# Optimization experiments

Hardware: AMD Instinct MI355X
Metric: run time of the kernel (lower is better)

## Reference

```python
import jax, jax.numpy as jnp
import numpy as np

D = 128      # d_model
H = 8        # heads
HD = D // H  # head dim
FF = 1024    # feedforward
L = 6        # encoder layers
LN_EPS = 1e-5


def setup_inputs() -> dict:
    key = jax.random.key(0)
    ks = jax.random.split(key, 10)
    S, B = 512, 64
    p = lambda k, shape: jax.random.normal(k, shape, dtype=jnp.float32) * 0.02
    return {
        "src": jax.random.normal(ks[0], (S, B, D), dtype=jnp.float32),
        "Wqkv": p(ks[1], (L, 3 * D, D)), "bqkv": p(ks[2], (L, 3 * D)),
        "Wo": p(ks[3], (L, D, D)), "bo": p(ks[4], (L, D)),
        "ln1_g": jnp.ones((L, D), jnp.float32), "ln1_b": jnp.zeros((L, D), jnp.float32),
        "W1": p(ks[5], (L, FF, D)), "b1": p(ks[6], (L, FF)),
        "W2": p(ks[7], (L, D, FF)), "b2": p(ks[8], (L, D)),
        "ln2_g": jnp.ones((L, D), jnp.float32), "ln2_b": jnp.zeros((L, D), jnp.float32),
    }


def _layer_norm(x, g, b):
    mu = jnp.mean(x, axis=-1, keepdims=True)
    var = jnp.mean(jnp.square(x - mu), axis=-1, keepdims=True)
    return (x - mu) * jax.lax.rsqrt(var + LN_EPS) * g + b


def _pairwise_cos(x):
    # x: (B, S, D) -> clamped cosine similarity (B, S, S); single batched GEMM
    n = jnp.linalg.norm(x, axis=-1)                      # (B, S)
    sim = jnp.einsum('bid,bjd->bij', x, x) / (n[:, :, None] * n[:, None, :])
    return jnp.maximum(sim, 1e-6)


def _encoder_layer(x, Wqkv, bqkv, Wo, bo, g1, b1ln, W1, b1, W2, b2, g2, b2ln):
    # x: (B, S, D); PyTorch post-norm TransformerEncoderLayer (ReLU), eval mode (no dropout)
    B, S, _ = x.shape
    qkv = x @ Wqkv.T + bqkv                              # (B, S, 3D)
    q, k, v = jnp.split(qkv, 3, axis=-1)
    q = q.reshape(B, S, H, HD)
    k = k.reshape(B, S, H, HD)
    v = v.reshape(B, S, H, HD)
    scores = jnp.einsum('bqhd,bkhd->bhqk', q, k) / np.float32(np.sqrt(HD))
    attn = jax.nn.softmax(scores, axis=-1)
    o = jnp.einsum('bhqk,bkhd->bqhd', attn, v).reshape(B, S, D)
    o = o @ Wo.T + bo
    x = _layer_norm(x + o, g1, b1ln)
    ff = jax.nn.relu(x @ W1.T + b1) @ W2.T + b2
    return _layer_norm(x + ff, g2, b2ln)


def reference(src, Wqkv, bqkv, Wo, bo, ln1_g, ln1_b, W1, b1, W2, b2, ln2_g, ln2_b):
    x_bsd = jnp.transpose(src, (1, 0, 2))                # (B, S, D)
    cs = _pairwise_cos(x_bsd)
    h = x_bsd
    for i in range(L):
        h = _encoder_layer(h, Wqkv[i], bqkv[i], Wo[i], bo[i], ln1_g[i], ln1_b[i],
                           W1[i], b1[i], W2[i], b2[i], ln2_g[i], ln2_b[i])
    mask = jax.nn.sigmoid(h)
    out = mask * x_bsd
    out = out / jnp.maximum(jnp.linalg.norm(out, axis=-1, keepdims=True), 1e-12)
    sim = _pairwise_cos(out) + cs
    return jnp.clip(sim * 0.5, 0.1, 0.9)
```

## Files before the change

### kernel.cpp

```cpp
#include <hip/hip_runtime.h>
#include <cstdint>
#include <cstddef>

#define SS 512
#define BB 64
#define DD 128
#define HH 8
#define HDIM 16
#define FFD 1024
#define NL 6

typedef short bf16x8 __attribute__((ext_vector_type(8)));
typedef float f32x4 __attribute__((ext_vector_type(4)));

__device__ inline uint32_t pack2(float a, float b) {
  uint32_t r;
  asm("v_cvt_pk_bf16_f32 %0, %1, %2" : "=v"(r) : "v"(a), "v"(b));
  return r;
}

#define QSCALE 0.36067376022224085f

__global__ __launch_bounds__(256) void cvt_kernel(const float* __restrict__ s,
                                                  short* __restrict__ d, int n2) {
  int i = blockIdx.x * 256 + threadIdx.x;
  if (i < n2) {
    float2 v = ((const float2*)s)[i];
    ((uint32_t*)d)[i] = pack2(v.x, v.y);
  }
}

__global__ __launch_bounds__(256) void cvt_qkv_kernel(const float* __restrict__ s,
                                                      short* __restrict__ d) {
  int i = blockIdx.x * 256 + threadIdx.x;
  if (i < NL * 384 * 64) {
    const int within = i % (384 * 64);
    const float sc = (within < 128 * 64) ? QSCALE : 1.0f;
    float2 v = ((const float2*)s)[i];
    ((uint32_t*)d)[i] = pack2(v.x * sc, v.y * sc);
  }
}

__global__ __launch_bounds__(256) void scale_bq_kernel(const float* __restrict__ s,
                                                       float* __restrict__ d) {
  int i = blockIdx.x * 256 + threadIdx.x;
  if (i < NL * 384) {
    const float sc = ((i % 384) < 128) ? QSCALE : 1.0f;
    d[i] = s[i] * sc;
  }
}

__global__ __launch_bounds__(256) void transpose_rn_kernel(const float* __restrict__ src,
                                                           float* __restrict__ x0,
                                                           float* __restrict__ h,
                                                           short* __restrict__ hb,
                                                           short* __restrict__ xn) {
  const int wave = threadIdx.x >> 6;
  const int lane = threadIdx.x & 63;
  const int row = blockIdx.x * 4 + wave;
  const int b = row >> 9;
  const int s = row & 511;
  const float2 v = ((const float2*)(src + ((size_t)s * BB + b) * DD))[lane];
  ((float2*)(x0 + (size_t)row * DD))[lane] = v;
  ((float2*)(h + (size_t)row * DD))[lane] = v;
  ((uint32_t*)hb)[(size_t)row * 64 + lane] = pack2(v.x, v.y);
  float ss = v.x * v.x + v.y * v.y;
  #pragma unroll
  for (int off = 1; off < 64; off <<= 1) ss += __shfl_xor(ss, off);
  const float r = rsqrtf(ss);
  ((uint32_t*)xn)[(size_t)row * 64 + lane] = pack2(v.x * r, v.y * r);
}

__global__ __launch_bounds__(256) void mgemm_qkv(const short* __restrict__ Ab,
                                                 const short* __restrict__ Bw,
                                                 const float* __restrict__ bias,
                                                 short* __restrict__ Cb) {
  __shared__ uint32_t Xs[128 * 32];
  __shared__ uint32_t Wls[128 * 32];
  const int t = threadIdx.x;
  const int wave = t >> 6, lane = t & 63;
  const int g = lane >> 4, p = lane & 15;
  const int wr = wave >> 1, wc = wave & 1;
  const int m0 = blockIdx.y * 128, n0 = blockIdx.x * 128;
  const int K = DD;

  f32x4 acc[4][4];
  #pragma unroll
  for (int i = 0; i < 4; ++i)
    #pragma unroll
    for (int j = 0; j < 4; ++j) acc[i][j] = (f32x4){0.f, 0.f, 0.f, 0.f};

  for (int kt = 0; kt < K; kt += 64) {
    __syncthreads();
    #pragma unroll
    for (int i = 0; i < 4; ++i) {
      const int idx = t + i * 256;
      const int row = idx >> 3, kc = idx & 7;
      const uint4 w = *(const uint4*)(Ab + (size_t)(m0 + row) * K + kt + kc * 8);
      *(uint4*)(Xs + row * 32 + ((kc ^ (row & 7)) << 2)) = w;
      const uint4 u = *(const uint4*)(Bw + (size_t)(n0 + row) * K + kt + kc * 8);
      *(uint4*)(Wls + row * 32 + ((kc ^ (row & 7)) << 2)) = u;
    }
    __syncthreads();
    #pragma unroll
    for (int kc32 = 0; kc32 < 2; ++kc32) {
      bf16x8 xf[4], wf[4];
      #pragma unroll
      for (int mi = 0; mi < 4; ++mi) {
        const int row = wr * 64 + mi * 16 + p;
        union { bf16x8 v; uint4 w; } u;
        u.w = *(const uint4*)(Xs + row * 32 + (((kc32 * 4 + g) ^ (row & 7)) << 2));
        xf[mi] = u.v;
      }
      #pragma unroll
      for (int ni = 0; ni < 4; ++ni) {
        const int row = wc * 64 + ni * 16 + p;
        union { bf16x8 v; uint4 w; } u;
        u.w = *(const uint4*)(Wls + row * 32 + (((kc32 * 4 + g) ^ (row & 7)) << 2));
        wf[ni] = u.v;
      }
      #pragma unroll
      for (int mi = 0; mi < 4; ++mi)
        #pragma unroll
        for (int ni = 0; ni < 4; ++ni)
          acc[mi][ni] = __builtin_amdgcn_mfma_f32_16x16x32_bf16(wf[ni], xf[mi], acc[mi][ni], 0, 0, 0);
    }
  }

  #pragma unroll
  for (int mi = 0; mi < 4; ++mi) {
    const int m = m0 + wr * 64 + mi * 16 + p;
    #pragma unroll
    for (int ni = 0; ni < 4; ++ni) {
      const int nb = n0 + wc * 64 + ni * 16 + g * 4;
      const float4 bv = *(const float4*)(bias + nb);
      float c[4];
      c[0] = acc[mi][ni][0] + bv.x;
      c[1] = acc[mi][ni][1] + bv.y;
      c[2] = acc[mi][ni][2] + bv.z;
      c[3] = acc[mi][ni][3] + bv.w;
      const int bb2 = m >> 9, s = m & 511;
      const int which = nb >> 7, hh = (nb >> 4) & 7, d = nb & 15;
      uint2 w;
      w.x = pack2(c[0], c[1]);
      w.y = pack2(c[2], c[3]);
      *(uint2*)(Cb + ((((size_t)(bb2 * 3 + which) * 8 + hh) * 512 + s) * 16 + d)) = w;
    }
  }
}

__global__ __launch_bounds__(256) void cos2_kernel(const short* __restrict__ xn,
                                                   const short* __restrict__ yn,
                                                   float* __restrict__ out) {
  __shared__ uint32_t Js[128 * 64];
  const int t = threadIdx.x;
  const int w = t >> 6, lane = t & 63;
  const int g = lane >> 4, p = lane & 15;
  const int j0 = blockIdx.x * 128;
  const int i0 = blockIdx.y * 64;
  const int b = blockIdx.z;
  const short* xb = xn + (size_t)b * SS * DD;
  const short* yb = yn + (size_t)b * SS * DD;
  const int i = i0 + w * 16 + p;

  bf16x8 af[4];
  #pragma unroll
  for (int kc = 0; kc < 4; ++kc) {
    union { bf16x8 v; uint4 u; } uu;
    uu.u = *(const uint4*)(xb + (size_t)i * DD + kc * 32 + g * 8);
    af[kc] = uu.v;
  }
  #pragma unroll
  for (int q = 0; q < 8; ++q) {
    const int idx = q * 256 + t;
    const int row = idx >> 4, slot = idx & 15;
    const int key = (row & 3) | ((row >> 1) & 12);
    const uint4 u = *(const uint4*)(xb + (size_t)(j0 + row) * DD + slot * 8);
    *(uint4*)(&Js[row * 64 + ((slot ^ key) << 2)]) = u;
  }
  __syncthreads();

  f32x4 acc[8];
  #pragma unroll
  for (int q = 0; q < 8; ++q) acc[q] = (f32x4){0.f, 0.f, 0.f, 0.f};
  #pragma unroll
  for (int kc = 0; kc < 4; ++kc) {
    #pragma unroll
    for (int ni = 0; ni < 8; ++ni) {
      const int row = ni * 16 + p;
      const int key = (row & 3) | ((row >> 1) & 12);
      union { bf16x8 v; uint4 u; } jf;
      jf.u = *(const uint4*)(&Js[row * 64 + (((kc * 4 + g) ^ key) << 2)]);
      acc[ni] = __builtin_amdgcn_mfma_f32_16x16x32_bf16(jf.v, af[kc], acc[ni], 0, 0, 0);
    }
  }
  float prev[8][4];
  #pragma unroll
  for (int ni = 0; ni < 8; ++ni)
    #pragma unroll
    for (int r = 0; r < 4; ++r) prev[ni][r] = fmaxf(acc[ni][r], 1e-6f);
  __syncthreads();

  #pragma unroll
  for (int kc = 0; kc < 4; ++kc) {
    union { bf16x8 v; uint4 u; } uu;
    uu.u = *(const uint4*)(yb + (size_t)i * DD + kc * 32 + g * 8);
    af[kc] = uu.v;
  }
  #pragma unroll
  for (int q = 0; q < 8; ++q) {
    const int idx = q * 256 + t;
    const int row = idx >> 4, slot = idx & 15;
    const int key = (row & 3) | ((row >> 1) & 12);
    const uint4 u = *(const uint4*)(yb + (size_t)(j0 + row) * DD + slot * 8);
    *(uint4*)(&Js[row * 64 + ((slot ^ key) << 2)]) = u;
  }
  __syncthreads();

  #pragma unroll
  for (int q = 0; q < 8; ++q) acc[q] = (f32x4){0.f, 0.f, 0.f, 0.f};
  #pragma unroll
  for (int kc = 0; kc < 4; ++kc) {
    #pragma unroll
    for (int ni = 0; ni < 8; ++ni) {
      const int row = ni * 16 + p;
      const int key = (row & 3) | ((row >> 1) & 12);
      union { bf16x8 v; uint4 u; } jf;
      jf.u = *(const uint4*)(&Js[row * 64 + (((kc * 4 + g) ^ key) << 2)]);
      acc[ni] = __builtin_amdgcn_mfma_f32_16x16x32_bf16(jf.v, af[kc], acc[ni], 0, 0, 0);
    }
  }

  float* ob = out + (size_t)b * SS * SS;
  #pragma unroll
  for (int ni = 0; ni < 8; ++ni) {
    const int j = j0 + ni * 16 + g * 4;
    float4 wv;
    float* pw = &wv.x;
    #pragma unroll
    for (int r = 0; r < 4; ++r) {
      const float v = fmaxf(acc[ni][r], 1e-6f);
      pw[r] = fminf(fmaxf(0.5f * (v + prev[ni][r]), 0.1f), 0.9f);
    }
    *(float4*)(ob + (size_t)i * SS + j) = wv;
  }
}

__global__ __launch_bounds__(256) void wo_ffn_ln_kernel(const short* __restrict__ att,
                                                        const short* __restrict__ Wob,
                                                        const float* __restrict__ bov,
                                                        const float* __restrict__ lng1,
                                                        const float* __restrict__ lnb1,
                                                        const short* __restrict__ W1b,
                                                        const float* __restrict__ b1v,
                                                        const short* __restrict__ W2b,
                                                        const float* __restrict__ b2v,
                                                        const float* __restrict__ lng2,
                                                        const float* __restrict__ lnb2,
                                                        float* __restrict__ hx,
                                                        short* __restrict__ hb,
                                                        const float* __restrict__ x0p,
                                                        short* __restrict__ ynp) {
  __shared__ uint32_t S[10240];
  uint32_t* WoLS = S;
  uint32_t* Tb   = S;
  uint32_t* W1base = S;
  uint32_t* W2base = S + 4096;
  const int t = threadIdx.x;
  const int w = t >> 6, lane = t & 63;
  const int g = lane >> 4, p = lane & 15;
  const int m0 = blockIdx.x * 64;
  const int m = m0 + w * 16 + p;
  const int lr = w * 16 + p;
  const int lkey = (lr & 3) | ((lr >> 1) & 12);

  bf16x8 af[4];
  #pragma unroll
  for (int kc = 0; kc < 4; ++kc) {
    union { bf16x8 v; uint4 u; } uu;
    uu.u = *(const uint4*)(att + (size_t)m * DD + kc * 32 + g * 8);
    af[kc] = uu.v;
  }
  #pragma unroll
  for (int i = 0; i < 8; ++i) {
    const int idx = i * 256 + t;
    const int row = idx >> 4, slot = idx & 15;
    const int key = (row & 3) | ((row >> 1) & 12);
    const uint4 u = *(const uint4*)(Wob + (size_t)row * DD + slot * 8);
    *(uint4*)(&WoLS[row * 64 + ((slot ^ key) << 2)]) = u;
  }
  __syncthreads();

  f32x4 acc[8];
  #pragma unroll
  for (int i = 0; i < 8; ++i) acc[i] = (f32x4){0.f, 0.f, 0.f, 0.f};
  #pragma unroll
  for (int kc = 0; kc < 4; ++kc) {
    #pragma unroll
    for (int ni = 0; ni < 8; ++ni) {
      const int row = ni * 16 + p;
      const int key = (row & 3) | ((row >> 1) & 12);
      union { bf16x8 v; uint4 u; } wf;
      wf.u = *(const uint4*)(&WoLS[row * 64 + (((kc * 4 + g) ^ key) << 2)]);
      acc[ni] = __builtin_amdgcn_mfma_f32_16x16x32_bf16(wf.v, af[kc], acc[ni], 0, 0, 0);
    }
  }

  float h1r[8][4];
  float s1r = 0.0f, s2r = 0.0f;
  #pragma unroll
  for (int ni = 0; ni < 8; ++ni) {
    const int nb = ni * 16 + g * 4;
    const float4 rv = *(const float4*)(hx + (size_t)m * DD + nb);
    const float4 bv = *(const float4*)(bov + nb);
    h1r[ni][0] = acc[ni][0] + bv.x + rv.x;
    h1r[ni][1] = acc[ni][1] + bv.y + rv.y;
    h1r[ni][2] = acc[ni][2] + bv.z + rv.z;
    h1r[ni][3] = acc[ni][3] + bv.w + rv.w;
    #pragma unroll
    for (int r = 0; r < 4; ++r) {
      s1r += h1r[ni][r];
      s2r += h1r[ni][r] * h1r[ni][r];
    }
  }
  s1r += __shfl_xor(s1r, 16); s1r += __shfl_xor(s1r, 32);
  s2r += __shfl_xor(s2r, 16); s2r += __shfl_xor(s2r, 32);
  {
    const float mu = s1r * (1.0f / 128.0f);
    const float rs = rsqrtf(fmaxf(s2r * (1.0f / 128.0f) - mu * mu, 0.0f) + 1e-5f);
    #pragma unroll
    for (int ni = 0; ni < 8; ++ni) {
      const int nb = ni * 16 + g * 4;
      const float4 gv = *(const float4*)(lng1 + nb);
      const float4 bv = *(const float4*)(lnb1 + nb);
      h1r[ni][0] = (h1r[ni][0] - mu) * rs * gv.x + bv.x;
      h1r[ni][1] = (h1r[ni][1] - mu) * rs * gv.y + bv.y;
      h1r[ni][2] = (h1r[ni][2] - mu) * rs * gv.z + bv.z;
      h1r[ni][3] = (h1r[ni][3] - mu) * rs * gv.w + bv.w;
    }
  }
  __syncthreads();

  #pragma unroll
  for (int ni = 0; ni < 8; ++ni) {
    const int w16 = ni * 8 + 2 * g;
    const int slot = w16 >> 2, offs = w16 & 3;
    uint2 pk;
    pk.x = pack2(h1r[ni][0], h1r[ni][1]);
    pk.y = pack2(h1r[ni][2], h1r[ni][3]);
    *(uint2*)(&Tb[lr * 64 + ((slot ^ lkey) << 2) + offs]) = pk;
  }
  __syncthreads();

  bf16x8 hsf[4];
  #pragma unroll
  for (int kc = 0; kc < 4; ++kc) {
    union { bf16x8 v; uint4 u; } uu;
    uu.u = *(const uint4*)(&Tb[lr * 64 + (((kc * 4 + g) ^ lkey) << 2)]);
    hsf[kc] = uu.v;
  }
  __syncthreads();

  uint4 rA0, rA1, rB0, rB1;

#define FFN_LOAD(c)                                                               \
  {                                                                               \
    const int nf0_ = (c) * 32;                                                    \
    rA0 = *(const uint4*)(W1b + (size_t)(nf0_ + (t >> 4)) * DD + (t & 15) * 8);   \
    rA1 = *(const uint4*)(W1b + (size_t)(nf0_ + 16 + (t >> 4)) * DD + (t & 15) * 8); \
    rB0 = *(const uint4*)(W2b + (size_t)(t >> 2) * FFD + nf0_ + (t & 3) * 8);     \
    rB1 = *(const uint4*)(W2b + (size_t)(64 + (t >> 2)) * FFD + nf0_ + (t & 3) * 8); \
  }

#define FFN_WRITE(bufA, bufB)                                                     \
  {                                                                               \
    uint32_t* W1p = W1base + (bufA) * 2048;                                       \
    uint32_t* W2p = W2base + (bufB) * 2048;                                       \
    const int rw0 = t >> 4, sl0 = t & 15;                                         \
    const int k0 = (rw0 & 3) | ((rw0 >> 1) & 12);                                 \
    *(uint4*)(&W1p[rw0 * 64 + ((sl0 ^ k0) << 2)]) = rA0;                          \
    const int rw1 = 16 + rw0;                                                     \
    const int k1 = (rw1 & 3) | ((rw1 >> 1) & 12);                                 \
    *(uint4*)(&W1p[rw1 * 64 + ((sl0 ^ k1) << 2)]) = rA1;                          \
    const int rw2 = t >> 2, sl2 = t & 3;                                          \
    *(uint4*)(&W2p[rw2 * 16 + ((sl2 ^ ((rw2 >> 1) & 3)) << 2)]) = rB0;            \
    const int rw3 = 64 + rw2;                                                     \
    *(uint4*)(&W2p[rw3 * 16 + ((sl2 ^ ((rw3 >> 1) & 3)) << 2)]) = rB1;            \
  }

  FFN_LOAD(0);
  FFN_WRITE(0, 0);
  __syncthreads();

  const int pr0 = 8 * (p >> 2) + (p & 3);
  const int pr1 = pr0 + 4;
  const int key0 = (pr0 & 3) | ((pr0 >> 1) & 12);
  const int key1 = (pr1 & 3) | ((pr1 >> 1) & 12);

  f32x4 acc2[8];
  #pragma unroll
  for (int i = 0; i < 8; ++i) acc2[i] = (f32x4){0.f, 0.f, 0.f, 0.f};
  const f32x4 zacc = {0.f, 0.f, 0.f, 0.f};

  bf16x8 pbv;
  int bPrev = 2, bCur = 0, bNext = 1;

  for (int c = 0; c < 32; ++c) {
    const int bA = c & 1;
    if (c + 1 < 32) FFN_LOAD(c + 1);

    const uint32_t* W1p = W1base + bA * 2048;
    f32x4 s0 = zacc, s1 = zacc;
    #pragma unroll
    for (int kc = 0; kc < 4; ++kc) {
      union { bf16x8 v; uint4 u; } a0, a1;
      a0.u = *(const uint4*)(&W1p[pr0 * 64 + (((kc * 4 + g) ^ key0) << 2)]);
      a1.u = *(const uint4*)(&W1p[pr1 * 64 + (((kc * 4 + g) ^ key1) << 2)]);
      s0 = __builtin_amdgcn_mfma_f32_16x16x32_bf16(a0.v, hsf[kc], s0, 0, 0, 0);
      s1 = __builtin_amdgcn_mfma_f32_16x16x32_bf16(a1.v, hsf[kc], s1, 0, 0, 0);
    }

    if (c > 0) {
      const uint32_t* W2p = W2base + bPrev * 2048;
      #pragma unroll
      for (int ni = 0; ni < 8; ++ni) {
        const int row = ni * 16 + p;
        union { bf16x8 v; uint4 u; } wf;
        wf.u = *(const uint4*)(&W2p[row * 16 + ((g ^ ((row >> 1) & 3)) << 2)]);
        acc2[ni] = __builtin_amdgcn_mfma_f32_16x16x32_bf16(wf.v, pbv, acc2[ni], 0, 0, 0);
      }
    }

    const int nf0 = c * 32;
    const float4 bb0 = *(const float4*)(b1v + nf0 + 8 * g);
    const float4 bb1 = *(const float4*)(b1v + nf0 + 8 * g + 4);
    union { bf16x8 v; uint4 u; } pb;
    pb.u.x = pack2(fmaxf(s0[0] + bb0.x, 0.0f), fmaxf(s0[1] + bb0.y, 0.0f));
    pb.u.y = pack2(fmaxf(s0[2] + bb0.z, 0.0f), fmaxf(s0[3] + bb0.w, 0.0f));
    pb.u.z = pack2(fmaxf(s1[0] + bb1.x, 0.0f), fmaxf(s1[1] + bb1.y, 0.0f));
    pb.u.w = pack2(fmaxf(s1[2] + bb1.z, 0.0f), fmaxf(s1[3] + bb1.w, 0.0f));
    pbv = pb.v;

    if (c + 1 < 32) FFN_WRITE(bA ^ 1, bNext);
    __syncthreads();

    bPrev = bCur; bCur = bNext; bNext = (bNext == 2) ? 0 : bNext + 1;
  }

  {
    const uint32_t* W2p = W2base + 1 * 2048;
    #pragma unroll
    for (int ni = 0; ni < 8; ++ni) {
      const int row = ni * 16 + p;
      union { bf16x8 v; uint4 u; } wf;
      wf.u = *(const uint4*)(&W2p[row * 16 + ((g ^ ((row >> 1) & 3)) << 2)]);
      acc2[ni] = __builtin_amdgcn_mfma_f32_16x16x32_bf16(wf.v, pbv, acc2[ni], 0, 0, 0);
    }
  }

  float t1 = 0.0f, t2 = 0.0f;
  #pragma unroll
  for (int ni = 0; ni < 8; ++ni) {
    const int nb = ni * 16 + g * 4;
    const float4 bv = *(const float4*)(b2v + nb);
    acc2[ni][0] += bv.x + h1r[ni][0];
    acc2[ni][1] += bv.y + h1r[ni][1];
    acc2[ni][2] += bv.z + h1r[ni][2];
    acc2[ni][3] += bv.w + h1r[ni][3];
    #pragma unroll
    for (int r = 0; r < 4; ++r) {
      t1 += acc2[ni][r];
      t2 += acc2[ni][r] * acc2[ni][r];
    }
  }
  t1 += __shfl_xor(t1, 16); t1 += __shfl_xor(t1, 32);
  t2 += __shfl_xor(t2, 16); t2 += __shfl_xor(t2, 32);
  const float mu2 = t1 * (1.0f / 128.0f);
  const float rs2 = rsqrtf(fmaxf(t2 * (1.0f / 128.0f) - mu2 * mu2, 0.0f) + 1e-5f);

  if (ynp == nullptr) {
    #pragma unroll
    for (int ni = 0; ni < 8; ++ni) {
      const int nb = ni * 16 + g * 4;
      const float4 gv = *(const float4*)(lng2 + nb);
      const float4 bv = *(const float4*)(lnb2 + nb);
      float c[4];
      c[0] = (acc2[ni][0] - mu2) * rs2 * gv.x + bv.x;
      c[1] = (acc2[ni][1] - mu2) * rs2 * gv.y + bv.y;
      c[2] = (acc2[ni][2] - mu2) * rs2 * gv.z + bv.z;
      c[3] = (acc2[ni][3] - mu2) * rs2 * gv.w + bv.w;
      float4 wv;
      wv.x = c[0]; wv.y = c[1]; wv.z = c[2]; wv.w = c[3];
      *(float4*)(hx + (size_t)m * DD + nb) = wv;
      uint2 wb;
      wb.x = pack2(c[0], c[1]);
      wb.y = pack2(c[2], c[3]);
      *(uint2*)(hb + (size_t)m * DD + nb) = wb;
    }
  } else {
    float av[8][4];
    float ssum = 0.0f;
    #pragma unroll
    for (int ni = 0; ni < 8; ++ni) {
      const int nb = ni * 16 + g * 4;
      const float4 gv = *(const float4*)(lng2 + nb);
      const float4 bv = *(const float4*)(lnb2 + nb);
      const float4 xv = *(const float4*)(x0p + (size_t)m * DD + nb);
      const float hc0 = (acc2[ni][0] - mu2) * rs2 * gv.x + bv.x;
      const float hc1 = (acc2[ni][1] - mu2) * rs2 * gv.y + bv.y;
      const float hc2 = (acc2[ni][2] - mu2) * rs2 * gv.z + bv.z;
      const float hc3 = (acc2[ni][3] - mu2) * rs2 * gv.w + bv.w;
      av[ni][0] = xv.x / (1.0f + __expf(-hc0));
      av[ni][1] = xv.y / (1.0f + __expf(-hc1));
      av[ni][2] = xv.z / (1.0f + __expf(-hc2));
      av[ni][3] = xv.w / (1.0f + __expf(-hc3));
      #pragma unroll
      for (int r = 0; r < 4; ++r) ssum += av[ni][r] * av[ni][r];
    }
    ssum += __shfl_xor(ssum, 16);
    ssum += __shfl_xor(ssum, 32);
    const float inv = 1.0f / fmaxf(sqrtf(ssum), 1e-12f);
    #pragma unroll
    for (int ni = 0; ni < 8; ++ni) {
      const int nb = ni * 16 + g * 4;
      uint2 wb;
      wb.x = pack2(av[ni][0] * inv, av[ni][1] * inv);
      wb.y = pack2(av[ni][2] * inv, av[ni][3] * inv);
      *(uint2*)(ynp + (size_t)m * DD + nb) = wb;
    }
  }
}

__global__ __launch_bounds__(512) void attn_mfma_kernel(const short* __restrict__ qkvp,
                                                        short* __restrict__ o_out) {
  const int h = blockIdx.x;
  const int b = blockIdx.y;
  const int z = blockIdx.z;
  const int t = threadIdx.x;
  const int wave = t >> 6;
  const int lane = t & 63;
  const int g = lane >> 4;
  const int p = lane & 15;

  __shared__ uint32_t Ks[512 * 8];
  __shared__ uint32_t Vs[16 * 256];

  const short* baseQ = qkvp + ((size_t)(b * 3 + 0) * 8 + h) * 8192;
  const short* baseK = qkvp + ((size_t)(b * 3 + 1) * 8 + h) * 8192;
  const short* baseV = qkvp + ((size_t)(b * 3 + 2) * 8 + h) * 8192;

  {
    const int row = t;
    const uint4 lo = *(const uint4*)(baseK + row * 16);
    const uint4 hi = *(const uint4*)(baseK + row * 16 + 8);
    const int f = ((row >> 3) & 1) << 2;
    *(uint4*)(Ks + row * 8 + f) = lo;
    *(uint4*)(Ks + row * 8 + (f ^ 4)) = hi;
  }
  {
    const int k = t;
    union { uint4 u[2]; short s[16]; } vv;
    vv.u[0] = *(const uint4*)(baseV + k * 16);
    vv.u[1] = *(const uint4*)(baseV + k * 16 + 8);
    const int wk = k >> 1;
    #pragma unroll
    for (int d = 0; d < 16; ++d) {
      const int word = d * 256 + (wk ^ ((d & 7) << 2));
      ((short*)(Vs + word))[k & 1] = vv.s[d];
    }
  }
  __syncthreads();

  const bf16x8 zfrag = {0, 0, 0, 0, 0, 0, 0, 0};
  const f32x4 zacc = {0.f, 0.f, 0.f, 0.f};

  #pragma unroll
  for (int qi = 0; qi < 2; ++qi) {
    const int qt = z * 16 + wave + qi * 8;
    bf16x8 qf = zfrag;
    if (g < 2) {
      union { bf16x8 v; uint4 w; } qu;
      qu.w = *(const uint4*)(baseQ + (qt * 16 + p) * 16 + g * 8);
      qf = qu.v;
    }

    f32x4 o = zacc;
    float lsum = 0.0f;

    for (int kv = 0; kv < 16; ++kv) {
      bf16x8 ka = zfrag, kb = zfrag;
      if (g < 2) {
        const int r0 = kv * 32 + 8 * (p >> 2) + (p & 3);
        const int r1 = r0 + 4;
        union { bf16x8 v; uint4 w; } u;
        u.w = *(const uint4*)(Ks + r0 * 8 + ((4 * g) ^ (((r0 >> 3) & 1) << 2)));
        ka = u.v;
        u.w = *(const uint4*)(Ks + r1 * 8 + ((4 * g) ^ (((r1 >> 3) & 1) << 2)));
        kb = u.v;
      }
      union { bf16x8 v; uint4 w; } vu;
      vu.w = *(const uint4*)(Vs + p * 256 + ((kv * 16 + g * 4) ^ ((p & 7) << 2)));

      const f32x4 s0 = __builtin_amdgcn_mfma_f32_16x16x32_bf16(ka, qf, zacc, 0, 0, 0);
      const f32x4 s1 = __builtin_amdgcn_mfma_f32_16x16x32_bf16(kb, qf, zacc, 0, 0, 0);

      float sv0[4], sv1[4];
      #pragma unroll
      for (int r = 0; r < 4; ++r) {
        sv0[r] = __builtin_amdgcn_exp2f(s0[r]);
        sv1[r] = __builtin_amdgcn_exp2f(s1[r]);
      }
      #pragma unroll
      for (int r = 0; r < 4; ++r) lsum += sv0[r] + sv1[r];

      union { bf16x8 v; uint4 w; } pu;
      pu.w.x = pack2(sv0[0], sv0[1]);
      pu.w.y = pack2(sv0[2], sv0[3]);
      pu.w.z = pack2(sv1[0], sv1[1]);
      pu.w.w = pack2(sv1[2], sv1[3]);

      o = __builtin_amdgcn_mfma_f32_16x16x32_bf16(pu.v, vu.v, o, 0, 0, 0);
    }

    lsum += __shfl_xor(lsum, 16);
    lsum += __shfl_xor(lsum, 32);
    const float li = 1.0f / lsum;
    #pragma unroll
    for (int r = 0; r < 4; ++r) {
      const float inv = __shfl(li, 4 * g + r);
      o_out[((size_t)(b * SS + qt * 16 + 4 * g + r)) * DD + h * HDIM + p] =
          (short)(pack2(o[r] * inv, 0.0f) & 0xffff);
    }
  }
}

extern "C" void kernel_launch(void* const* d_in, const int* in_sizes, int n_in,
                              void* d_out, int out_size, void* d_ws, size_t ws_size,
                              hipStream_t stream) {
  const float* src  = (const float*)d_in[0];
  const float* Wqkv = (const float*)d_in[1];
  const float* bqkv = (const float*)d_in[2];
  const float* Wo   = (const float*)d_in[3];
  const float* bo   = (const float*)d_in[4];
  const float* ln1g = (const float*)d_in[5];
  const float* ln1b = (const float*)d_in[6];
  const float* W1   = (const float*)d_in[7];
  const float* b1   = (const float*)d_in[8];
  const float* W2   = (const float*)d_in[9];
  const float* b2   = (const float*)d_in[10];
  const float* ln2g = (const float*)d_in[11];
  const float* ln2b = (const float*)d_in[12];
  float* out = (float*)d_out;

  char* W = (char*)d_ws;
  const size_t MB = 1048576;
  float* x0  = (float*)(W);
  float* h   = (float*)(W + 16 * MB);
  short* hb  = (short*)(W + 32 * MB);
  short* qkvp = (short*)(W + 40 * MB);
  short* att = (short*)(W + 128 * MB);
  short* xn  = (short*)(W + 136 * MB);
  short* yn  = (short*)(W + 144 * MB);
  short* wqB = (short*)(W + 152 * MB);
  short* woB = wqB + (size_t)NL * 384 * DD;
  short* w1B = woB + (size_t)NL * DD * DD;
  short* w2B = w1B + (size_t)NL * FFD * DD;
  float* bq2 = (float*)(w2B + (size_t)NL * DD * FFD);

  const dim3 blk(256);
  const int ROWS = BB * SS;

  cvt_qkv_kernel<<<(NL * 384 * 64 + 255) / 256, blk, 0, stream>>>(Wqkv, wqB);
  cvt_kernel<<<(NL * DD * DD / 2 + 255) / 256, blk, 0, stream>>>(Wo, woB, NL * DD * DD / 2);
  cvt_kernel<<<(NL * FFD * DD / 2 + 255) / 256, blk, 0, stream>>>(W1, w1B, NL * FFD * DD / 2);
  cvt_kernel<<<(NL * DD * FFD / 2 + 255) / 256, blk, 0, stream>>>(W2, w2B, NL * DD * FFD / 2);
  scale_bq_kernel<<<(NL * 384 + 255) / 256, blk, 0, stream>>>(bqkv, bq2);

  transpose_rn_kernel<<<ROWS / 4, blk, 0, stream>>>(src, x0, h, hb, xn);

  for (int l = 0; l < NL; ++l) {
    mgemm_qkv<<<dim3(3, ROWS / 128), blk, 0, stream>>>(
        hb, wqB + (size_t)l * 384 * DD, bq2 + l * 384, qkvp);
    attn_mfma_kernel<<<dim3(HH, BB, 2), dim3(512), 0, stream>>>(qkvp, att);
    const bool last = (l == NL - 1);
    wo_ffn_ln_kernel<<<dim3(ROWS / 64), blk, 0, stream>>>(
        att, woB + (size_t)l * DD * DD, bo + l * DD, ln1g + l * DD, ln1b + l * DD,
        w1B + (size_t)l * FFD * DD, b1 + l * FFD,
        w2B + (size_t)l * DD * FFD, b2 + l * DD,
        ln2g + l * DD, ln2b + l * DD, h, hb,
        last ? x0 : nullptr, last ? yn : nullptr);
  }

  cos2_kernel<<<dim3(4, 8, BB), blk, 0, stream>>>(xn, yn, out);
}
```

Measured before the change: 522.1 us.

## Fuse next layer's QKV projection into the Wo/FFN/LayerNorm kernel epilogue

Layers after the first no longer launch a separate QKV GEMM. The fused Wo+FFN+LN kernel now stages its LayerNorm output as bf16 in shared memory, then multiplies it by the next layer's Wqkv, streamed in double-buffered 32-row chunks, and writes the head-major qkv buffer directly. This removes the bf16 hidden-state write and re-read and five kernel launches. In exchange, the fused kernel gets longer and carries more register and shared-memory pressure, and each 64-row block must reload all of Wqkv.

```diff
diff --git a/kernel.cpp b/kernel.cpp
--- a/kernel.cpp
+++ b/kernel.cpp
@@ -258,7 +258,9 @@
                                                         const float* __restrict__ lng2,
                                                         const float* __restrict__ lnb2,
                                                         float* __restrict__ hx,
-                                                        short* __restrict__ hb,
+                                                        const short* __restrict__ Wqn,
+                                                        const float* __restrict__ bqn,
+                                                        short* __restrict__ qkvo,
                                                         const float* __restrict__ x0p,
                                                         short* __restrict__ ynp) {
   __shared__ uint32_t S[10240];
@@ -478,26 +480,7 @@
   const float mu2 = t1 * (1.0f / 128.0f);
   const float rs2 = rsqrtf(fmaxf(t2 * (1.0f / 128.0f) - mu2 * mu2, 0.0f) + 1e-5f);
 
-  if (ynp == nullptr) {
-    #pragma unroll
-    for (int ni = 0; ni < 8; ++ni) {
-      const int nb = ni * 16 + g * 4;
-      const float4 gv = *(const float4*)(lng2 + nb);
-      const float4 bv = *(const float4*)(lnb2 + nb);
-      float c[4];
-      c[0] = (acc2[ni][0] - mu2) * rs2 * gv.x + bv.x;
-      c[1] = (acc2[ni][1] - mu2) * rs2 * gv.y + bv.y;
-      c[2] = (acc2[ni][2] - mu2) * rs2 * gv.z + bv.z;
-      c[3] = (acc2[ni][3] - mu2) * rs2 * gv.w + bv.w;
-      float4 wv;
-      wv.x = c[0]; wv.y = c[1]; wv.z = c[2]; wv.w = c[3];
-      *(float4*)(hx + (size_t)m * DD + nb) = wv;
-      uint2 wb;
-      wb.x = pack2(c[0], c[1]);
-      wb.y = pack2(c[2], c[3]);
-      *(uint2*)(hb + (size_t)m * DD + nb) = wb;
-    }
-  } else {
+  if (ynp != nullptr) {
     float av[8][4];
     float ssum = 0.0f;
     #pragma unroll
@@ -528,6 +511,95 @@
       wb.y = pack2(av[ni][2] * inv, av[ni][3] * inv);
       *(uint2*)(ynp + (size_t)m * DD + nb) = wb;
     }
+    return;
+  }
+
+  #pragma unroll
+  for (int ni = 0; ni < 8; ++ni) {
+    const int nb = ni * 16 + g * 4;
+    const float4 gv = *(const float4*)(lng2 + nb);
+    const float4 bv = *(const float4*)(lnb2 + nb);
+    h1r[ni][0] = (acc2[ni][0] - mu2) * rs2 * gv.x + bv.x;
+    h1r[ni][1] = (acc2[ni][1] - mu2) * rs2 * gv.y + bv.y;
+    h1r[ni][2] = (acc2[ni][2] - mu2) * rs2 * gv.z + bv.z;
+    h1r[ni][3] = (acc2[ni][3] - mu2) * rs2 * gv.w + bv.w;
+    float4 wv;
+    wv.x = h1r[ni][0]; wv.y = h1r[ni][1]; wv.z = h1r[ni][2]; wv.w = h1r[ni][3];
+    *(float4*)(hx + (size_t)m * DD + nb) = wv;
+  }
+
+  #pragma unroll
+  for (int ni = 0; ni < 8; ++ni) {
+    const int w16 = ni * 8 + 2 * g;
+    const int slot = w16 >> 2, offs = w16 & 3;
+    uint2 pk;
+    pk.x = pack2(h1r[ni][0], h1r[ni][1]);
+    pk.y = pack2(h1r[ni][2], h1r[ni][3]);
+    *(uint2*)(&Tb[lr * 64 + ((slot ^ lkey) << 2) + offs]) = pk;
+  }
+  __syncthreads();
+
+  #pragma unroll
+  for (int kc = 0; kc < 4; ++kc) {
+    union { bf16x8 v; uint4 u; } uu;
+    uu.u = *(const uint4*)(&Tb[lr * 64 + (((kc * 4 + g) ^ lkey) << 2)]);
+    hsf[kc] = uu.v;
+  }
+  __syncthreads();
+
+#define QKV_LOAD(c)                                                               \
+  {                                                                               \
+    const int nf0_ = (c) * 32;                                                    \
+    rA0 = *(const uint4*)(Wqn + (size_t)(nf0_ + (t >> 4)) * DD + (t & 15) * 8);   \
+    rA1 = *(const uint4*)(Wqn + (size_t)(nf0_ + 16 + (t >> 4)) * DD + (t & 15) * 8); \
+  }
+
+#define QKV_WRITE(bufA)                                                           \
+  {                                                                               \
+    uint32_t* W1p = W1base + (bufA) * 2048;                                       \
+    const int rw0 = t >> 4, sl0 = t & 15;                                         \
+    const int k0 = (rw0 & 3) | ((rw0 >> 1) & 12);                                 \
+    *(uint4*)(&W1p[rw0 * 64 + ((sl0 ^ k0) << 2)]) = rA0;                          \
+    const int rw1 = 16 + rw0;                                                     \
+    const int k1 = (rw1 & 3) | ((rw1 >> 1) & 12);                                 \
+    *(uint4*)(&W1p[rw1 * 64 + ((sl0 ^ k1) << 2)]) = rA1;                          \
+  }
+
+  QKV_LOAD(0);
+  QKV_WRITE(0);
+  __syncthreads();
+
+  const int bb2 = m >> 9, sm = m & 511;
+  for (int c = 0; c < 12; ++c) {
+    const int bA = c & 1;
+    if (c + 1 < 12) QKV_LOAD(c + 1);
+
+    const uint32_t* W1p = W1base + bA * 2048;
+    f32x4 s0 = zacc, s1 = zacc;
+    #pragma unroll
+    for (int kc = 0; kc < 4; ++kc) {
+      union { bf16x8 v; uint4 u; } a0, a1;
+      a0.u = *(const uint4*)(&W1p[pr0 * 64 + (((kc * 4 + g) ^ key0) << 2)]);
+      a1.u = *(const uint4*)(&W1p[pr1 * 64 + (((kc * 4 + g) ^ key1) << 2)]);
+      s0 = __builtin_amdgcn_mfma_f32_16x16x32_bf16(a0.v, hsf[kc], s0, 0, 0, 0);
+      s1 = __builtin_amdgcn_mfma_f32_16x16x32_bf16(a1.v, hsf[kc], s1, 0, 0, 0);
+    }
+
+    const int n0q = c * 32 + 8 * g;
+    const float4 b0 = *(const float4*)(bqn + n0q);
+    const float4 b4 = *(const float4*)(bqn + n0q + 4);
+    const int which = n0q >> 7, hh = (n0q >> 4) & 7, d0 = n0q & 15;
+    short* base = qkvo + ((((size_t)(bb2 * 3 + which) * 8 + hh) * 512 + sm) * 16 + d0);
+    uint2 w0, w1;
+    w0.x = pack2(s0[0] + b0.x, s0[1] + b0.y);
+    w0.y = pack2(s0[2] + b0.z, s0[3] + b0.w);
+    w1.x = pack2(s1[0] + b4.x, s1[1] + b4.y);
+    w1.y = pack2(s1[2] + b4.z, s1[3] + b4.w);
+    *(uint2*)(base) = w0;
+    *(uint2*)(base + 4) = w1;
+
+    if (c + 1 < 12) QKV_WRITE(bA ^ 1);
+    __syncthreads();
   }
 }
 
@@ -678,16 +750,19 @@
 
   transpose_rn_kernel<<<ROWS / 4, blk, 0, stream>>>(src, x0, h, hb, xn);
 
+  mgemm_qkv<<<dim3(3, ROWS / 128), blk, 0, stream>>>(hb, wqB, bq2, qkvp);
+
   for (int l = 0; l < NL; ++l) {
-    mgemm_qkv<<<dim3(3, ROWS / 128), blk, 0, stream>>>(
-        hb, wqB + (size_t)l * 384 * DD, bq2 + l * 384, qkvp);
     attn_mfma_kernel<<<dim3(HH, BB, 2), dim3(512), 0, stream>>>(qkvp, att);
     const bool last = (l == NL - 1);
     wo_ffn_ln_kernel<<<dim3(ROWS / 64), blk, 0, stream>>>(
         att, woB + (size_t)l * DD * DD, bo + l * DD, ln1g + l * DD, ln1b + l * DD,
         w1B + (size_t)l * FFD * DD, b1 + l * FFD,
         w2B + (size_t)l * DD * FFD, b2 + l * DD,
-        ln2g + l * DD, ln2b + l * DD, h, hb,
+        ln2g + l * DD, ln2b + l * DD, h,
+        last ? nullptr : (wqB + (size_t)(l + 1) * 384 * DD),
+        last ? nullptr : (bq2 + (l + 1) * 384),
+        last ? nullptr : qkvp,
         last ? x0 : nullptr, last ? yn : nullptr);
   }
 
```

After: 500.3 us. 1.04x faster.
